# Optimization experiments

Measured on AMD Instinct MI355X. Metric: run time of the kernel, lower is better.

## Reference

```python
import jax, jax.numpy as jnp
import numpy as np
from jax import lax

D_MODEL = 1024
D_STATE = 16


def setup_inputs() -> dict:
    key = jax.random.key(0)
    ks = jax.random.split(key, 7)
    B, L = 4, 2048
    x = jax.random.normal(ks[0], (B, L, D_MODEL), dtype=jnp.float32)
    s = 1.0 / np.sqrt(D_MODEL)
    W_dt = jax.random.uniform(ks[1], (D_MODEL, D_MODEL), jnp.float32, -s, s)
    b_dt = jax.random.uniform(ks[2], (D_MODEL,), jnp.float32, -s, s)
    W_B = jax.random.uniform(ks[3], (D_STATE, D_MODEL), jnp.float32, -s, s)
    W_C = jax.random.uniform(ks[4], (D_STATE, D_MODEL), jnp.float32, -s, s)
    A = jax.random.normal(ks[5], (D_MODEL, D_STATE), dtype=jnp.float32)
    A_log = jnp.log(jnp.abs(A) + 1e-4)
    D = jnp.ones((D_MODEL,), dtype=jnp.float32)
    return {"x": x, "W_dt": W_dt, "b_dt": b_dt, "W_B": W_B, "W_C": W_C,
            "A_log": A_log, "D": D}


def reference(x, W_dt, b_dt, W_B, W_C, A_log, D):
    B, L, Dm = x.shape
    N = A_log.shape[1]
    dt = jax.nn.softplus(jnp.einsum('bld,ed->ble', x, W_dt) + b_dt)  # [B,L,D]
    Bp = jnp.einsum('bld,nd->bln', x, W_B)   # [B,L,N]
    Cp = jnp.einsum('bld,nd->bln', x, W_C)   # [B,L,N]
    A = -jnp.exp(A_log)                      # [D,N]
    dA = jnp.exp(dt[..., None] * A)          # [B,L,D,N]
    # fuse dB * x: dB[bldn] = dt*Bp; input term = dB * x
    dBx = dt[..., None] * Bp[:, :, None, :] * x[..., None]  # [B,L,D,N]

    def step(h, inp):
        dA_t, dBx_t, C_t, x_t = inp
        h = dA_t * h + dBx_t                              # [B,D,N]
        y = jnp.einsum('bdn,bn->bd', h, C_t) + D * x_t    # [B,D]
        return h, y

    h0 = jnp.zeros((B, Dm, N), dtype=x.dtype)
    xs = (jnp.swapaxes(dA, 0, 1), jnp.swapaxes(dBx, 0, 1),
          jnp.swapaxes(Cp, 0, 1), jnp.swapaxes(x, 0, 1))
    _, ys = lax.scan(step, h0, xs)           # ys: [L,B,D]
    return jnp.swapaxes(ys, 0, 1)            # [B,L,D]
```

## Files before the change

kernel.cpp:

```cpp
#include <hip/hip_runtime.h>
#include <hip/hip_bf16.h>
#include <math.h>

#define DM 1024
#define DS 16
#define BB 4
#define LL 2048
#define LC 32
#define NC (LL/LC)
#define MT 8192
#define NT 32
#define NCT 17

typedef __attribute__((ext_vector_type(8))) short short8;
typedef __attribute__((ext_vector_type(4))) float floatx4;

__device__ __forceinline__ float softplus_fast(float v) {
  return fmaxf(v, 0.f) + __logf(1.f + __expf(-fabsf(v)));
}

__global__ __launch_bounds__(256) void convert_kernel(
    const float* __restrict__ X, const float* __restrict__ W_dt,
    const float* __restrict__ WB, const float* __restrict__ WC,
    __hip_bfloat16* __restrict__ Xb, __hip_bfloat16* __restrict__ Wx)
{
  const size_t i  = (size_t)blockIdx.x * 256 + threadIdx.x;
  const size_t NX = (size_t)MT * DM / 8;
  const size_t NW = (size_t)DM * DM / 8;
  const size_t NB = (size_t)DS * DM / 8;
  const float* src;
  __hip_bfloat16* dst;
  size_t u;
  if (i < NX)                { src = X;    dst = Xb;                        u = i; }
  else if (i < NX + NW)      { src = W_dt; dst = Wx;                        u = i - NX; }
  else if (i < NX + NW + NB) { src = WB;   dst = Wx + (size_t)1024 * DM;    u = i - NX - NW; }
  else if (i < NX + NW + 2 * NB) { src = WC; dst = Wx + (size_t)1040 * DM;  u = i - NX - NW - NB; }
  else {
    const size_t z = i - NX - NW - 2 * NB;
    const short8 zz = {0, 0, 0, 0, 0, 0, 0, 0};
    *(short8*)&Wx[(size_t)1056 * DM + z * 8] = zz;
    return;
  }
  const float4 a = *(const float4*)&src[u * 8];
  const float4 b = *(const float4*)&src[u * 8 + 4];
  union { short8 v; __hip_bfloat16 h[8]; } o;
  o.h[0] = __float2bfloat16(a.x); o.h[1] = __float2bfloat16(a.y);
  o.h[2] = __float2bfloat16(a.z); o.h[3] = __float2bfloat16(a.w);
  o.h[4] = __float2bfloat16(b.x); o.h[5] = __float2bfloat16(b.y);
  o.h[6] = __float2bfloat16(b.z); o.h[7] = __float2bfloat16(b.w);
  *(short8*)&dst[u * 8] = o.v;
}

__global__ __launch_bounds__(256) void gemm_dt_mfma(
    const __hip_bfloat16* __restrict__ Xb, const __hip_bfloat16* __restrict__ Wx,
    const float* __restrict__ bias, __hip_bfloat16* __restrict__ DTb,
    float* __restrict__ BP, float* __restrict__ CP)
{
  __shared__ short As[3][128 * 32];
  __shared__ short Bs[3][64 * 32];
  const int tid  = threadIdx.x;
  const int lane = tid & 63;
  const int wid  = tid >> 6;
  const int wm   = wid >> 1, wn = wid & 1;

  const int bid  = blockIdx.x;
  const int tile = (bid & 7) * 136 + (bid >> 3);
  const int row0 = (tile / NCT) * 128;
  const int col0 = (tile % NCT) * 64;

  const floatx4 zero = {0.f, 0.f, 0.f, 0.f};
  floatx4 acc[4][2];
#pragma unroll
  for (int i = 0; i < 4; ++i)
#pragma unroll
    for (int j = 0; j < 2; ++j) acc[i][j] = zero;

  auto STAGE = [&](int buf, int t) {
    const int k0 = t * 32;
#pragma unroll
    for (int q = 0; q < 2; ++q) {
      const int fe = q * 256 + tid;
      const int r  = fe >> 2;
      const int kk = (fe & 3) * 8;
      __builtin_amdgcn_global_load_lds(
          (const __attribute__((address_space(1))) void*)&Xb[(size_t)(row0 + r) * DM + k0 + kk],
          (__attribute__((address_space(3))) void*)&As[buf][fe * 8], 16, 0, 0);
    }
    const int rb  = tid >> 2;
    const int kkb = (tid & 3) * 8;
    __builtin_amdgcn_global_load_lds(
        (const __attribute__((address_space(1))) void*)&Wx[(size_t)(col0 + rb) * DM + k0 + kkb],
        (__attribute__((address_space(3))) void*)&Bs[buf][tid * 8], 16, 0, 0);
  };

  STAGE(0, 0);
  STAGE(1, 1);
  int cur = 0;
  for (int t = 0; t < NT; ++t) {
    if (t < NT - 1) asm volatile("s_waitcnt vmcnt(3)" ::: "memory");
    else            asm volatile("s_waitcnt vmcnt(0)" ::: "memory");
    __builtin_amdgcn_s_barrier();
    __builtin_amdgcn_sched_barrier(0);

    int c2 = cur + 2; if (c2 >= 3) c2 -= 3;
    if (t + 2 < NT) STAGE(c2, t + 2);

    short8 af[4], bfr[2];
#pragma unroll
    for (int i = 0; i < 4; ++i) {
      const int ar = wm * 64 + i * 16 + (lane & 15);
      af[i] = *(const short8*)&As[cur][ar * 32 + (lane >> 4) * 8];
    }
#pragma unroll
    for (int j = 0; j < 2; ++j) {
      const int br = wn * 32 + j * 16 + (lane & 15);
      bfr[j] = *(const short8*)&Bs[cur][br * 32 + (lane >> 4) * 8];
    }
#pragma unroll
    for (int i = 0; i < 4; ++i)
#pragma unroll
      for (int j = 0; j < 2; ++j)
        acc[i][j] = __builtin_amdgcn_mfma_f32_16x16x32_bf16(af[i], bfr[j], acc[i][j], 0, 0, 0);

    cur += 1; if (cur >= 3) cur -= 3;
  }

  const int cl = lane & 15;
  const int rg = lane >> 4;
  if (col0 < 1024) {
#pragma unroll
    for (int i = 0; i < 4; ++i) {
#pragma unroll
      for (int r = 0; r < 4; ++r) {
        const size_t row = (size_t)(row0 + wm * 64 + i * 16 + rg * 4 + r);
#pragma unroll
        for (int j = 0; j < 2; ++j) {
          const int col = col0 + wn * 32 + j * 16 + cl;
          const float v = acc[i][j][r] + bias[col];
          DTb[row * DM + col] = __float2bfloat16(softplus_fast(v));
        }
      }
    }
  } else if (wn == 0) {
#pragma unroll
    for (int i = 0; i < 4; ++i) {
#pragma unroll
      for (int r = 0; r < 4; ++r) {
        const size_t row = (size_t)(row0 + wm * 64 + i * 16 + rg * 4 + r);
        BP[row * DS + cl] = acc[i][0][r];
        CP[row * DS + cl] = acc[i][1][r];
      }
    }
  }
}

__global__ __launch_bounds__(256) void scan_partial_kernel(
    const __hip_bfloat16* __restrict__ DT, const __hip_bfloat16* __restrict__ X,
    const float* __restrict__ Bp, const float* __restrict__ A_log,
    float* __restrict__ PP, float* __restrict__ HP)
{
  const int d = blockIdx.x * 256 + threadIdx.x;
  const int c = blockIdx.y;
  const int b = blockIdx.z;
  float A[DS], h[DS];
  float sdt = 0.f;
  const float4* arow = (const float4*)&A_log[(size_t)d * DS];
#pragma unroll
  for (int m = 0; m < 4; ++m) {
    const float4 a4 = arow[m];
    A[m*4+0] = -__expf(a4.x); A[m*4+1] = -__expf(a4.y);
    A[m*4+2] = -__expf(a4.z); A[m*4+3] = -__expf(a4.w);
  }
#pragma unroll
  for (int n = 0; n < DS; ++n) h[n] = 0.f;

  const int l0 = c * LC;
  size_t idx = ((size_t)b * LL + l0) * DM + d;
  const float4* bv = (const float4*)&Bp[((size_t)b * LL + l0) * DS];

  float dtb[4], xb[4];
#pragma unroll
  for (int u = 0; u < 4; ++u) {
    dtb[u] = __bfloat162float(DT[idx + (size_t)u * DM]);
    xb[u]  = __bfloat162float(X[idx + (size_t)u * DM]);
  }

  for (int l = 0; l < LC; l += 4) {
    float dtn[4], xn[4];
    if (l + 4 < LC) {
#pragma unroll
      for (int u = 0; u < 4; ++u) {
        dtn[u] = __bfloat162float(DT[idx + (size_t)(u + 4) * DM]);
        xn[u]  = __bfloat162float(X[idx + (size_t)(u + 4) * DM]);
      }
    }
#pragma unroll
    for (int u = 0; u < 4; ++u) {
      const float dtv = dtb[u], xv = xb[u];
      const float dx = dtv * xv;
      sdt += dtv;
      const float4 b0 = bv[(l+u)*4+0], b1 = bv[(l+u)*4+1];
      const float4 b2 = bv[(l+u)*4+2], b3 = bv[(l+u)*4+3];
      const float bb[DS] = {b0.x,b0.y,b0.z,b0.w, b1.x,b1.y,b1.z,b1.w,
                            b2.x,b2.y,b2.z,b2.w, b3.x,b3.y,b3.z,b3.w};
#pragma unroll
      for (int n = 0; n < DS; ++n) {
        const float dA = __expf(dtv * A[n]);
        h[n] = fmaf(dA, h[n], dx * bb[n]);
      }
    }
    idx += (size_t)4 * DM;
#pragma unroll
    for (int u = 0; u < 4; ++u) { dtb[u] = dtn[u]; xb[u] = xn[u]; }
  }
  const size_t o = (((size_t)b * NC + c) * DM + d) * DS;
  float4* pp = (float4*)&PP[o];
  float4* hp = (float4*)&HP[o];
#pragma unroll
  for (int m = 0; m < 4; ++m) {
    pp[m] = make_float4(__expf(sdt * A[m*4+0]), __expf(sdt * A[m*4+1]),
                        __expf(sdt * A[m*4+2]), __expf(sdt * A[m*4+3]));
    hp[m] = make_float4(h[m*4+0], h[m*4+1], h[m*4+2], h[m*4+3]);
  }
}

__global__ __launch_bounds__(256) void combine_kernel(
    float* __restrict__ PP, const float* __restrict__ HP)
{
  const int idx = blockIdx.x * 256 + threadIdx.x;
  const int b  = idx >> 14;
  const int dn = idx & 16383;
  float h = 0.f;
#pragma unroll 4
  for (int c = 0; c < NC; ++c) {
    const size_t o = (((size_t)b * NC + c) << 14) + dn;
    const float p  = PP[o];
    const float hp = HP[o];
    PP[o] = h;
    h = fmaf(p, h, hp);
  }
}

__global__ __launch_bounds__(256) void scan_final_kernel(
    const __hip_bfloat16* __restrict__ DT, const __hip_bfloat16* __restrict__ X,
    const float* __restrict__ Bp, const float* __restrict__ Cp,
    const float* __restrict__ A_log, const float* __restrict__ Dvec,
    const float* __restrict__ Hin, float* __restrict__ Y)
{
  const int d = blockIdx.x * 256 + threadIdx.x;
  const int c = blockIdx.y;
  const int b = blockIdx.z;
  float A[DS], h[DS];
  const float4* arow = (const float4*)&A_log[(size_t)d * DS];
  const size_t o = (((size_t)b * NC + c) * DM + d) * DS;
  const float4* hin = (const float4*)&Hin[o];
#pragma unroll
  for (int m = 0; m < 4; ++m) {
    const float4 a4 = arow[m];
    A[m*4+0] = -__expf(a4.x); A[m*4+1] = -__expf(a4.y);
    A[m*4+2] = -__expf(a4.z); A[m*4+3] = -__expf(a4.w);
    const float4 h4 = hin[m];
    h[m*4+0] = h4.x; h[m*4+1] = h4.y; h[m*4+2] = h4.z; h[m*4+3] = h4.w;
  }
  const float Dd = Dvec[d];
  const int l0 = c * LC;
  size_t idx = ((size_t)b * LL + l0) * DM + d;
  const float4* bv = (const float4*)&Bp[((size_t)b * LL + l0) * DS];
  const float4* cv = (const float4*)&Cp[((size_t)b * LL + l0) * DS];

  float dtb[4], xb[4];
#pragma unroll
  for (int u = 0; u < 4; ++u) {
    dtb[u] = __bfloat162float(DT[idx + (size_t)u * DM]);
    xb[u]  = __bfloat162float(X[idx + (size_t)u * DM]);
  }

  for (int l = 0; l < LC; l += 4) {
    float dtn[4], xn[4];
    if (l + 4 < LC) {
#pragma unroll
      for (int u = 0; u < 4; ++u) {
        dtn[u] = __bfloat162float(DT[idx + (size_t)(u + 4) * DM]);
        xn[u]  = __bfloat162float(X[idx + (size_t)(u + 4) * DM]);
      }
    }
#pragma unroll
    for (int u = 0; u < 4; ++u) {
      const float dtv = dtb[u], xv = xb[u];
      const float dx = dtv * xv;
      const float4 b0 = bv[(l+u)*4+0], b1 = bv[(l+u)*4+1];
      const float4 b2 = bv[(l+u)*4+2], b3 = bv[(l+u)*4+3];
      const float bb[DS] = {b0.x,b0.y,b0.z,b0.w, b1.x,b1.y,b1.z,b1.w,
                            b2.x,b2.y,b2.z,b2.w, b3.x,b3.y,b3.z,b3.w};
      const float4 c0 = cv[(l+u)*4+0], c1 = cv[(l+u)*4+1];
      const float4 c2 = cv[(l+u)*4+2], c3 = cv[(l+u)*4+3];
      const float cc[DS] = {c0.x,c0.y,c0.z,c0.w, c1.x,c1.y,c1.z,c1.w,
                            c2.x,c2.y,c2.z,c2.w, c3.x,c3.y,c3.z,c3.w};
      float y = 0.f;
#pragma unroll
      for (int n = 0; n < DS; ++n) {
        const float dA = __expf(dtv * A[n]);
        h[n] = fmaf(dA, h[n], dx * bb[n]);
        y = fmaf(h[n], cc[n], y);
      }
      Y[idx + (size_t)u * DM] = fmaf(Dd, xv, y);
    }
    idx += (size_t)4 * DM;
#pragma unroll
    for (int u = 0; u < 4; ++u) { dtb[u] = dtn[u]; xb[u] = xn[u]; }
  }
}

extern "C" void kernel_launch(void* const* d_in, const int* in_sizes, int n_in,
                              void* d_out, int out_size, void* d_ws, size_t ws_size,
                              hipStream_t stream)
{
  const float* x     = (const float*)d_in[0];
  const float* W_dt  = (const float*)d_in[1];
  const float* b_dt  = (const float*)d_in[2];
  const float* W_B   = (const float*)d_in[3];
  const float* W_C   = (const float*)d_in[4];
  const float* A_log = (const float*)d_in[5];
  const float* Dv    = (const float*)d_in[6];
  float* Y  = (float*)d_out;
  float* ws = (float*)d_ws;

  __hip_bfloat16* DTb = (__hip_bfloat16*)ws;
  float* BP = ws + (size_t)MT * DM / 2;
  float* CP = BP + (size_t)MT * DS;
  __hip_bfloat16* Xb = (__hip_bfloat16*)(CP + (size_t)MT * DS);
  float* U  = CP + (size_t)MT * DS + (size_t)MT * DM / 2;
  __hip_bfloat16* Wx = (__hip_bfloat16*)U;
  float* PP = U;
  float* HP = U + (size_t)BB * NC * DM * DS;

  convert_kernel<<<4640, 256, 0, stream>>>(x, W_dt, W_B, W_C, Xb, Wx);
  gemm_dt_mfma<<<1088, 256, 0, stream>>>(Xb, Wx, b_dt, DTb, BP, CP);
  scan_partial_kernel<<<dim3(DM / 256, NC, BB), 256, 0, stream>>>(DTb, Xb, BP, A_log, PP, HP);
  combine_kernel<<<(BB * DM * DS) / 256, 256, 0, stream>>>(PP, HP);
  scan_final_kernel<<<dim3(DM / 256, NC, BB), 256, 0, stream>>>(DTb, Xb, BP, CP, A_log, Dv, PP, Y);
}
```

Before: 143.4 us.

## Load GEMM fragments directly to registers and recompute chunk decay in combine

The GEMM drops its LDS triple-buffered staging. Each wave now loads its MFMA fragments straight from global memory into registers, double-buffered in software, with no barriers. The scan partial pass writes one summed dt per (b,c,d) instead of 16 decay products, and the combine kernel recomputes exp(sdt*A) from that, shrinking intermediate traffic by about 16x for that array. The price is redundant global loads in the GEMM, since there is no LDS sharing across waves, so it leans on L2/L1 for reuse, plus extra exps in the combine kernel.

```diff
diff --git a/kernel.cpp b/kernel.cpp
--- a/kernel.cpp
+++ b/kernel.cpp
@@ -56,8 +56,6 @@
     const float* __restrict__ bias, __hip_bfloat16* __restrict__ DTb,
     float* __restrict__ BP, float* __restrict__ CP)
 {
-  __shared__ short As[3][128 * 32];
-  __shared__ short Bs[3][64 * 32];
   const int tid  = threadIdx.x;
   const int lane = tid & 63;
   const int wid  = tid >> 6;
@@ -68,6 +66,11 @@
   const int row0 = (tile / NCT) * 128;
   const int col0 = (tile % NCT) * 64;
 
+  const int fr = lane & 15;
+  const int ks = lane >> 4;
+  const __hip_bfloat16* pa = &Xb[(size_t)(row0 + wm * 64 + fr) * DM + ks * 8];
+  const __hip_bfloat16* pb = &Wx[(size_t)(col0 + wn * 32 + fr) * DM + ks * 8];
+
   const floatx4 zero = {0.f, 0.f, 0.f, 0.f};
   floatx4 acc[4][2];
 #pragma unroll
@@ -75,54 +78,35 @@
 #pragma unroll
     for (int j = 0; j < 2; ++j) acc[i][j] = zero;
 
-  auto STAGE = [&](int buf, int t) {
-    const int k0 = t * 32;
-#pragma unroll
-    for (int q = 0; q < 2; ++q) {
-      const int fe = q * 256 + tid;
-      const int r  = fe >> 2;
-      const int kk = (fe & 3) * 8;
-      __builtin_amdgcn_global_load_lds(
-          (const __attribute__((address_space(1))) void*)&Xb[(size_t)(row0 + r) * DM + k0 + kk],
-          (__attribute__((address_space(3))) void*)&As[buf][fe * 8], 16, 0, 0);
-    }
-    const int rb  = tid >> 2;
-    const int kkb = (tid & 3) * 8;
-    __builtin_amdgcn_global_load_lds(
-        (const __attribute__((address_space(1))) void*)&Wx[(size_t)(col0 + rb) * DM + k0 + kkb],
-        (__attribute__((address_space(3))) void*)&Bs[buf][tid * 8], 16, 0, 0);
+  short8 a0[4], b0[2], a1[4], b1[2];
+
+  auto LOAD0 = [&](int t) {
+#pragma unroll
+    for (int i = 0; i < 4; ++i) a0[i] = *(const short8*)&pa[(size_t)(i * 16) * DM + t * 32];
+#pragma unroll
+    for (int j = 0; j < 2; ++j) b0[j] = *(const short8*)&pb[(size_t)(j * 16) * DM + t * 32];
   };
-
-  STAGE(0, 0);
-  STAGE(1, 1);
-  int cur = 0;
-  for (int t = 0; t < NT; ++t) {
-    if (t < NT - 1) asm volatile("s_waitcnt vmcnt(3)" ::: "memory");
-    else            asm volatile("s_waitcnt vmcnt(0)" ::: "memory");
-    __builtin_amdgcn_s_barrier();
-    __builtin_amdgcn_sched_barrier(0);
-
-    int c2 = cur + 2; if (c2 >= 3) c2 -= 3;
-    if (t + 2 < NT) STAGE(c2, t + 2);
-
-    short8 af[4], bfr[2];
-#pragma unroll
-    for (int i = 0; i < 4; ++i) {
-      const int ar = wm * 64 + i * 16 + (lane & 15);
-      af[i] = *(const short8*)&As[cur][ar * 32 + (lane >> 4) * 8];
-    }
-#pragma unroll
-    for (int j = 0; j < 2; ++j) {
-      const int br = wn * 32 + j * 16 + (lane & 15);
-      bfr[j] = *(const short8*)&Bs[cur][br * 32 + (lane >> 4) * 8];
-    }
+  auto LOAD1 = [&](int t) {
+#pragma unroll
+    for (int i = 0; i < 4; ++i) a1[i] = *(const short8*)&pa[(size_t)(i * 16) * DM + t * 32];
+#pragma unroll
+    for (int j = 0; j < 2; ++j) b1[j] = *(const short8*)&pb[(size_t)(j * 16) * DM + t * 32];
+  };
+
+  LOAD0(0);
+  for (int t = 0; t < NT; t += 2) {
+    LOAD1(t + 1);
 #pragma unroll
     for (int i = 0; i < 4; ++i)
 #pragma unroll
       for (int j = 0; j < 2; ++j)
-        acc[i][j] = __builtin_amdgcn_mfma_f32_16x16x32_bf16(af[i], bfr[j], acc[i][j], 0, 0, 0);
-
-    cur += 1; if (cur >= 3) cur -= 3;
+        acc[i][j] = __builtin_amdgcn_mfma_f32_16x16x32_bf16(a0[i], b0[j], acc[i][j], 0, 0, 0);
+    if (t + 2 < NT) LOAD0(t + 2);
+#pragma unroll
+    for (int i = 0; i < 4; ++i)
+#pragma unroll
+      for (int j = 0; j < 2; ++j)
+        acc[i][j] = __builtin_amdgcn_mfma_f32_16x16x32_bf16(a1[i], b1[j], acc[i][j], 0, 0, 0);
   }
 
   const int cl = lane & 15;
@@ -157,7 +141,7 @@
 __global__ __launch_bounds__(256) void scan_partial_kernel(
     const __hip_bfloat16* __restrict__ DT, const __hip_bfloat16* __restrict__ X,
     const float* __restrict__ Bp, const float* __restrict__ A_log,
-    float* __restrict__ PP, float* __restrict__ HP)
+    float* __restrict__ SD, float* __restrict__ HP)
 {
   const int d = blockIdx.x * 256 + threadIdx.x;
   const int c = blockIdx.y;
@@ -213,30 +197,30 @@
 #pragma unroll
     for (int u = 0; u < 4; ++u) { dtb[u] = dtn[u]; xb[u] = xn[u]; }
   }
+  SD[((size_t)b * NC + c) * DM + d] = sdt;
   const size_t o = (((size_t)b * NC + c) * DM + d) * DS;
-  float4* pp = (float4*)&PP[o];
   float4* hp = (float4*)&HP[o];
 #pragma unroll
-  for (int m = 0; m < 4; ++m) {
-    pp[m] = make_float4(__expf(sdt * A[m*4+0]), __expf(sdt * A[m*4+1]),
-                        __expf(sdt * A[m*4+2]), __expf(sdt * A[m*4+3]));
+  for (int m = 0; m < 4; ++m)
     hp[m] = make_float4(h[m*4+0], h[m*4+1], h[m*4+2], h[m*4+3]);
-  }
 }
 
 __global__ __launch_bounds__(256) void combine_kernel(
-    float* __restrict__ PP, const float* __restrict__ HP)
+    const float* __restrict__ SD, const float* __restrict__ A_log,
+    float* HP)
 {
   const int idx = blockIdx.x * 256 + threadIdx.x;
   const int b  = idx >> 14;
   const int dn = idx & 16383;
+  const int d  = dn >> 4;
+  const float A = -__expf(A_log[dn]);
   float h = 0.f;
 #pragma unroll 4
   for (int c = 0; c < NC; ++c) {
     const size_t o = (((size_t)b * NC + c) << 14) + dn;
-    const float p  = PP[o];
+    const float p  = __expf(SD[((size_t)b * NC + c) * DM + d] * A);
     const float hp = HP[o];
-    PP[o] = h;
+    HP[o] = h;
     h = fmaf(p, h, hp);
   }
 }
@@ -329,14 +313,13 @@
   float* BP = ws + (size_t)MT * DM / 2;
   float* CP = BP + (size_t)MT * DS;
   __hip_bfloat16* Xb = (__hip_bfloat16*)(CP + (size_t)MT * DS);
-  float* U  = CP + (size_t)MT * DS + (size_t)MT * DM / 2;
-  __hip_bfloat16* Wx = (__hip_bfloat16*)U;
-  float* PP = U;
-  float* HP = U + (size_t)BB * NC * DM * DS;
+  __hip_bfloat16* Wx = (__hip_bfloat16*)(CP + (size_t)MT * DS + (size_t)MT * DM / 2);
+  float* SD = CP + (size_t)MT * DS + (size_t)MT * DM / 2 + (size_t)1088 * DM / 2;
+  float* HP = SD + (size_t)BB * NC * DM;
 
   convert_kernel<<<4640, 256, 0, stream>>>(x, W_dt, W_B, W_C, Xb, Wx);
   gemm_dt_mfma<<<1088, 256, 0, stream>>>(Xb, Wx, b_dt, DTb, BP, CP);
-  scan_partial_kernel<<<dim3(DM / 256, NC, BB), 256, 0, stream>>>(DTb, Xb, BP, A_log, PP, HP);
-  combine_kernel<<<(BB * DM * DS) / 256, 256, 0, stream>>>(PP, HP);
-  scan_final_kernel<<<dim3(DM / 256, NC, BB), 256, 0, stream>>>(DTb, Xb, BP, CP, A_log, Dv, PP, Y);
-}
+  scan_partial_kernel<<<dim3(DM / 256, NC, BB), 256, 0, stream>>>(DTb, Xb, BP, A_log, SD, HP);
+  combine_kernel<<<(BB * DM * DS) / 256, 256, 0, stream>>>(SD, A_log, HP);
+  scan_final_kernel<<<dim3(DM / 256, NC, BB), 256, 0, stream>>>(DTb, Xb, BP, CP, A_log, Dv, HP, Y);
+}
```

Measured after the change: 203.6 us. 1.42x slower.
